# Kernel tuning notes

Hardware: AMD Instinct MI355X
Metric: run time of the kernel (lower is better)

## Reference

```python
import jax, jax.numpy as jnp
import numpy as np

B, T, D, S, K = 8, 4096, 1024, 64, 3
EPS = 1e-5

def setup_inputs() -> dict:
    key = jax.random.key(0)
    ks = jax.random.split(key, 10)
    def lin(k, out_d, in_d):
        s = 1.0 / np.sqrt(in_d)
        return jax.random.uniform(k, (out_d, in_d), jnp.float32, -s, s)
    return {
        "x": jax.random.normal(ks[0], (B, T, D), jnp.float32),
        "norm_w": jnp.ones((D,), jnp.float32),
        "norm_b": jnp.zeros((D,), jnp.float32),
        "in_w": lin(ks[1], 2 * D, D),
        "in_b": jnp.zeros((2 * D,), jnp.float32),
        "conv_w": jax.random.normal(ks[2], (D, 1, K), jnp.float32) / np.sqrt(K),
        "conv_b": jnp.zeros((D,), jnp.float32),
        "dt_w": lin(ks[3], S, D),
        "dt_b": jnp.zeros((S,), jnp.float32),
        "b_w": lin(ks[4], S, D),
        "b_b": jnp.zeros((S,), jnp.float32),
        "c_w": lin(ks[5], S, D),
        "c_b": jnp.zeros((S,), jnp.float32),
        "a_log": jax.random.normal(ks[6], (S,), jnp.float32) * 0.02,
        "d": jnp.ones((D,), jnp.float32),
        "out_w": lin(ks[7], D, D + S),
        "out_b": jnp.zeros((D,), jnp.float32),
    }

def reference(x, norm_w, norm_b, in_w, in_b, conv_w, conv_b,
              dt_w, dt_b, b_w, b_b, c_w, c_b, a_log, d, out_w, out_b):
    bsz, tlen, dim = x.shape
    sdim = a_log.shape[0]
    k = conv_w.shape[-1]
    residual = x
    # LayerNorm
    mu = jnp.mean(x, axis=-1, keepdims=True)
    var = jnp.mean(jnp.square(x - mu), axis=-1, keepdims=True)
    xn = (x - mu) * jax.lax.rsqrt(var + EPS) * norm_w + norm_b
    # in_proj and chunk
    h = xn @ in_w.T + in_b                       # (B,T,2D)
    x_proj, z = jnp.split(h, 2, axis=-1)         # each (B,T,D)
    # depthwise conv over time, 'same' padding
    xc = jax.lax.conv_general_dilated(
        x_proj.transpose(0, 2, 1), conv_w, (1,), [(k // 2, k // 2)],
        dimension_numbers=("NCH", "OIH", "NCH"), feature_group_count=dim)
    x_conv = jnp.tanh((xc + conv_b[None, :, None]).transpose(0, 2, 1))  # (B,T,D)
    # gate projections for all timesteps at once
    dt = jax.nn.softplus(z @ dt_w.T + dt_b) + 1e-4   # (B,T,S)
    b = jnp.tanh(z @ b_w.T + b_b)                    # (B,T,S)
    c = jnp.tanh(z @ c_w.T + c_b)                    # (B,T,S)
    a = -jnp.exp(a_log)                              # (S,)
    decay = jnp.exp(a * dt)                          # (B,T,S)
    # linear recurrence: state_t = state_{t-1} * decay_t + b_t
    def step(state, inp):
        dec_t, b_t = inp
        state = state * dec_t + b_t
        return state, state
    _, states = jax.lax.scan(step, jnp.zeros((bsz, sdim), x.dtype),
                             (decay.transpose(1, 0, 2), b.transpose(1, 0, 2)))
    states = states.transpose(1, 0, 2)               # (B,T,S)
    y = c * states
    mix = jnp.concatenate([x_conv * d, y], axis=-1)  # (B,T,D+S)
    out = mix @ out_w.T + out_b                      # (B,T,D)
    return residual + out
```

## Files before the change

### kernel.cpp

```cpp
#include <hip/hip_runtime.h>

#define TT 4096
#define DD 1024
#define NN 32768

typedef short s16x8 __attribute__((ext_vector_type(8)));
typedef float f32x4 __attribute__((ext_vector_type(4)));
typedef unsigned short ushort_t;

__device__ __forceinline__ unsigned short f2bf(float f) {
  unsigned u = __float_as_uint(f);
  u += 0x7FFFu + ((u >> 16) & 1u);
  return (unsigned short)(u >> 16);
}
__device__ __forceinline__ float bf2f(unsigned short h) {
  return __uint_as_float(((unsigned)h) << 16);
}
__device__ __forceinline__ void load_lds16(const void* g, void* l) {
  __builtin_amdgcn_global_load_lds(
      (const __attribute__((address_space(1))) unsigned int*)g,
      (__attribute__((address_space(3))) unsigned int*)l, 16, 0, 0);
}

__global__ __launch_bounds__(256)
void cvt_kernel(const float* __restrict__ s, ushort_t* __restrict__ d, int n) {
  int i = (blockIdx.x * 256 + threadIdx.x) * 4;
  if (i < n) {
    float4 v = *(const float4*)&s[i];
    ushort4 o; o.x = f2bf(v.x); o.y = f2bf(v.y); o.z = f2bf(v.z); o.w = f2bf(v.w);
    *(ushort4*)&d[i] = o;
  }
}

__global__ __launch_bounds__(256)
void w3pad_kernel(const float* __restrict__ dt_w, const float* __restrict__ b_w,
                  const float* __restrict__ c_w, ushort_t* __restrict__ w3) {
  int e = (blockIdx.x * 256 + threadIdx.x) * 4;
  int row = e >> 10, col = e & 1023;
  float4 v; v.x = 0.f; v.y = 0.f; v.z = 0.f; v.w = 0.f;
  if (row < 64)       v = *(const float4*)&dt_w[(row << 10) + col];
  else if (row < 128) v = *(const float4*)&b_w[((row - 64) << 10) + col];
  else if (row < 192) v = *(const float4*)&c_w[((row - 128) << 10) + col];
  ushort4 o; o.x = f2bf(v.x); o.y = f2bf(v.y); o.z = f2bf(v.z); o.w = f2bf(v.w);
  *(ushort4*)&w3[e] = o;
}

__global__ __launch_bounds__(256)
void tpose_kernel(const float* __restrict__ src, ushort_t* __restrict__ dst) {
  __shared__ float tile[64][65];
  int bx = blockIdx.x & 15, by = blockIdx.x >> 4;
  int tx = threadIdx.x & 63, ty0 = threadIdx.x >> 6;
  #pragma unroll
  for (int i = 0; i < 16; ++i) {
    int ty = ty0 * 16 + i;
    tile[ty][tx] = src[(size_t)(by * 64 + ty) * 1024 + bx * 64 + tx];
  }
  __syncthreads();
  #pragma unroll
  for (int i = 0; i < 16; ++i) {
    int ty = ty0 * 16 + i;
    dst[(size_t)(bx * 64 + ty) * 1024 + by * 64 + tx] = f2bf(tile[tx][ty]);
  }
}

__global__ void gbias_kernel(const float* __restrict__ dt_w, const float* __restrict__ b_w,
                             const float* __restrict__ c_w, const float* __restrict__ dt_b,
                             const float* __restrict__ b_b, const float* __restrict__ c_b,
                             const float* __restrict__ in_b, float* __restrict__ gb) {
  int i = blockIdx.x, lane = threadIdx.x;
  const float* wr = i < 64 ? dt_w + (size_t)i * 1024
                  : i < 128 ? b_w + (size_t)(i - 64) * 1024
                            : c_w + (size_t)(i - 128) * 1024;
  float s = 0.f;
  for (int j = lane; j < 1024; j += 64) s += wr[j] * in_b[1024 + j];
  #pragma unroll
  for (int off = 32; off; off >>= 1) s += __shfl_xor(s, off, 64);
  if (lane == 0) {
    float bb = i < 64 ? dt_b[i] : i < 128 ? b_b[i - 64] : c_b[i - 128];
    gb[i] = s + bb;
  }
}

__global__ __launch_bounds__(256)
void ln_kernel(const float* __restrict__ x, const float* __restrict__ w,
               const float* __restrict__ bv, ushort_t* __restrict__ xn)
{
  int row = blockIdx.x * 4 + (threadIdx.x >> 6);
  int lane = threadIdx.x & 63;
  const float* xr = x + (size_t)row * DD;
  float4 v[4];
  float s = 0.f, ss = 0.f;
  #pragma unroll
  for (int j = 0; j < 4; ++j) {
    v[j] = *(const float4*)&xr[j * 256 + lane * 4];
    s  += v[j].x + v[j].y + v[j].z + v[j].w;
    ss += v[j].x * v[j].x + v[j].y * v[j].y + v[j].z * v[j].z + v[j].w * v[j].w;
  }
  #pragma unroll
  for (int off = 32; off > 0; off >>= 1) {
    s  += __shfl_xor(s, off, 64);
    ss += __shfl_xor(ss, off, 64);
  }
  float mean = s * (1.f / 1024.f);
  float var  = ss * (1.f / 1024.f) - mean * mean;
  float rinv = rsqrtf(var + 1e-5f);
  #pragma unroll
  for (int j = 0; j < 4; ++j) {
    int c = j * 256 + lane * 4;
    float4 wv = *(const float4*)&w[c];
    float4 bb = *(const float4*)&bv[c];
    ushort4 o;
    o.x = f2bf((v[j].x - mean) * rinv * wv.x + bb.x);
    o.y = f2bf((v[j].y - mean) * rinv * wv.y + bb.y);
    o.z = f2bf((v[j].z - mean) * rinv * wv.z + bb.z);
    o.w = f2bf((v[j].w - mean) * rinv * wv.w + bb.w);
    *(ushort4*)&xn[(size_t)row * DD + c] = o;
  }
}

template<int EP>
__global__ __launch_bounds__(512, 2)
void gemm256(const ushort_t* __restrict__ A, const ushort_t* __restrict__ W,
             int M, int N, int K,
             const float* __restrict__ bias0,
             ushort_t* __restrict__ o0, ushort_t* __restrict__ o1)
{
  __shared__ ushort_t lds[65536];
  const int tid = threadIdx.x;
  const int lane = tid & 63;
  const int wid = tid >> 6;
  const int wr = wid >> 2;
  const int wc = wid & 3;
  const int lane15 = lane & 15;
  const int lgrp = lane >> 4;
  const int rsw = (lane15 & 7) << 4;
  const int ntn = N >> 8;
  int bid = blockIdx.x;
  { const int cpx = (int)gridDim.x >> 3; bid = (bid & 7) * cpx + (bid >> 3); }
  const int brow = (bid / ntn) << 8;
  const int bcol = (bid % ntn) << 8;
  const int nk = K >> 6;
  const int sRow = tid >> 3;
  const int sCol = (tid & 7) << 4;
  const char* ldsb = (const char*)lds;
  (void)M;

#define STG(bufb, isB, h, kt) do { \
    const int ktc_ = (kt) < nk ? (kt) : nk - 1; \
    const ushort_t* gsrc_ = (isB) ? W : A; \
    const int rowb_ = ((isB) ? bcol : brow) + (h) * 128; \
    _Pragma("unroll") \
    for (int j_ = 0; j_ < 2; ++j_) { \
      const int r_ = j_ * 64 + sRow; \
      load_lds16((const char*)(gsrc_ + (size_t)(rowb_ + r_) * K) + ktc_ * 128 + (sCol ^ ((r_ & 7) << 4)), \
                 (char*)lds + (bufb) * 65536 + (isB) * 32768 + (h) * 16384 + r_ * 128 + sCol); \
    } } while (0)

#define LDA_(bufb, m, kk) \
  (*(const s16x8*)(ldsb + (bufb) * 65536 + wr * 16384 + ((m) * 16 + lane15) * 128 + (((kk) * 64 + lgrp * 16) ^ rsw)))
#define LDB_(bufb, n, kk) \
  (*(const s16x8*)(ldsb + (bufb) * 65536 + 32768 + (wc >> 1) * 16384 + ((wc & 1) * 64 + (n) * 16 + lane15) * 128 + (((kk) * 64 + lgrp * 16) ^ rsw)))

#define BARR() asm volatile("s_barrier" ::: "memory")
#define VMW2() asm volatile("s_waitcnt vmcnt(2)" ::: "memory")
#define VMW4() asm volatile("s_waitcnt vmcnt(4)" ::: "memory")

#define RDA(dst, bufb, mh) do { \
    _Pragma("unroll") for (int kk = 0; kk < 2; ++kk) \
    _Pragma("unroll") for (int q = 0; q < 4; ++q) \
      dst[kk][q] = LDA_(bufb, (mh) * 4 + q, kk); } while (0)
#define RDB(dst, bufb, nh) do { \
    _Pragma("unroll") for (int kk = 0; kk < 2; ++kk) \
    _Pragma("unroll") for (int p = 0; p < 2; ++p) \
      dst[kk][p] = LDB_(bufb, (nh) * 2 + p, kk); } while (0)

#define MFMAQ(AF, BF, mh, nh) do { \
    __builtin_amdgcn_s_setprio(1); \
    _Pragma("unroll") for (int kk = 0; kk < 2; ++kk) \
    _Pragma("unroll") for (int q = 0; q < 4; ++q) \
    _Pragma("unroll") for (int p = 0; p < 2; ++p) \
      acc[(mh) * 4 + q][(nh) * 2 + p] = __builtin_amdgcn_mfma_f32_16x16x32_bf16( \
          AF[kk][q], BF[kk][p], acc[(mh) * 4 + q][(nh) * 2 + p], 0, 0, 0); \
    __builtin_amdgcn_s_setprio(0); } while (0)

  f32x4 acc[8][4];
  #pragma unroll
  for (int m = 0; m < 8; ++m) {
    #pragma unroll
    for (int n = 0; n < 4; ++n) acc[m][n] = (f32x4){0.f, 0.f, 0.f, 0.f};
  }
  s16x8 afP[2][4], afQ[2][4];
  s16x8 b0[2][2], b1[2][2];

  STG(0, 1, 0, 0); STG(0, 0, 0, 0); STG(0, 0, 1, 0); STG(0, 1, 1, 0);
  STG(1, 1, 0, 1); STG(1, 0, 0, 1);
  VMW4(); BARR();
  RDA(afP, 0, 0); RDB(b0, 0, 0);

  const int nIter = nk >> 1;
  for (int it = 0; it < nIter; ++it) {
    const int t0 = 2 * it;
    STG(1, 0, 1, t0 + 1);
    MFMAQ(afP, b0, 0, 0);
    RDB(b1, 0, 1); BARR();
    STG(1, 1, 1, t0 + 1);
    MFMAQ(afP, b1, 0, 1);
    RDA(afQ, 0, 1); BARR();
    STG(0, 1, 0, t0 + 2);
    MFMAQ(afQ, b1, 1, 1);
    VMW2(); BARR();
    STG(0, 0, 0, t0 + 2);
    MFMAQ(afQ, b0, 1, 0);
    RDA(afP, 1, 0); RDB(b1, 1, 1); BARR();
    STG(0, 0, 1, t0 + 2);
    MFMAQ(afP, b1, 0, 1);
    RDB(b0, 1, 0); BARR();
    STG(0, 1, 1, t0 + 2);
    MFMAQ(afP, b0, 0, 0);
    RDA(afQ, 1, 1); BARR();
    STG(1, 1, 0, t0 + 3);
    MFMAQ(afQ, b0, 1, 0);
    VMW2(); BARR();
    STG(1, 0, 0, t0 + 3);
    MFMAQ(afQ, b1, 1, 1);
    RDA(afP, 0, 0); RDB(b0, 0, 0); BARR();
  }
  if (nk & 1) {
    MFMAQ(afP, b0, 0, 0);
    RDB(b1, 0, 1);
    MFMAQ(afP, b1, 0, 1);
    RDA(afQ, 0, 1);
    MFMAQ(afQ, b1, 1, 1);
    MFMAQ(afQ, b0, 1, 0);
  }

#undef STG
#undef LDA_
#undef LDB_
#undef BARR
#undef VMW2
#undef VMW4
#undef RDA
#undef RDB
#undef MFMAQ

  #pragma unroll
  for (int m = 0; m < 8; ++m) {
    #pragma unroll
    for (int i = 0; i < 4; ++i) {
      const int r = brow + wr * 128 + m * 16 + lgrp * 4 + i;
      #pragma unroll
      for (int n = 0; n < 4; ++n) {
        const int col = bcol + wc * 64 + n * 16 + lane15;
        float v = acc[m][n][i] + bias0[col];
        if (col < DD) o0[(size_t)r * DD + col] = f2bf(v);
        else          o1[(size_t)r * DD + (col - DD)] = f2bf(v);
      }
    }
  }
}

__global__ __launch_bounds__(512, 4)
void gemm3_bk32(const ushort_t* __restrict__ A, const ushort_t* __restrict__ W,
                int M, int N, int K,
                const float* __restrict__ bias, const float* __restrict__ resid,
                float* __restrict__ outf)
{
  __shared__ ushort_t lds[24576];
  const int tid = threadIdx.x;
  const int lane = tid & 63;
  const int wid = tid >> 6;
  const int wr = wid >> 2;
  const int wc = wid & 3;
  const int lane15 = lane & 15;
  const int lgrp = lane >> 4;
  const int ntn = N >> 8;
  int bid = blockIdx.x;
  { const int cpx = (int)gridDim.x >> 3; bid = (bid & 7) * cpx + (bid >> 3); }
  const int brow = (bid / ntn) << 7;
  const int bcol = (bid % ntn) << 8;
  const int nk = K >> 5;
  const int sR = tid >> 2;
  const int sC = (tid & 3) << 4;
  const char* ldsb = (const char*)lds;
  (void)M;

  f32x4 acc[4][4];
  #pragma unroll
  for (int q = 0; q < 4; ++q)
    #pragma unroll
    for (int p = 0; p < 4; ++p) acc[q][p] = (f32x4){0.f, 0.f, 0.f, 0.f};

#define STG3(bufb, kt) do { \
    load_lds16((const char*)(A + (size_t)(brow + sR) * K + (kt) * 32) + sC, \
               (char*)lds + (bufb) * 24576 + sR * 64 + sC); \
    load_lds16((const char*)(W + (size_t)(bcol + sR) * K + (kt) * 32) + sC, \
               (char*)lds + (bufb) * 24576 + 8192 + sR * 64 + sC); \
    load_lds16((const char*)(W + (size_t)(bcol + 128 + sR) * K + (kt) * 32) + sC, \
               (char*)lds + (bufb) * 24576 + 8192 + (128 + sR) * 64 + sC); \
  } while (0)

  STG3(0, 0);
  __syncthreads();

  int cur = 0;
  for (int t = 0; t < nk; ++t) {
    if (t + 1 < nk) STG3(cur ^ 1, t + 1);
    s16x8 af[4], bf[4];
    #pragma unroll
    for (int q = 0; q < 4; ++q)
      af[q] = *(const s16x8*)(ldsb + cur * 24576 + (wr * 64 + q * 16 + lane15) * 64 + lgrp * 16);
    #pragma unroll
    for (int p = 0; p < 4; ++p)
      bf[p] = *(const s16x8*)(ldsb + cur * 24576 + 8192 + (wc * 64 + p * 16 + lane15) * 64 + lgrp * 16);
    __builtin_amdgcn_s_setprio(1);
    #pragma unroll
    for (int q = 0; q < 4; ++q)
      #pragma unroll
      for (int p = 0; p < 4; ++p)
        acc[q][p] = __builtin_amdgcn_mfma_f32_16x16x32_bf16(af[q], bf[p], acc[q][p], 0, 0, 0);
    __builtin_amdgcn_s_setprio(0);
    __syncthreads();
    cur ^= 1;
  }
#undef STG3

  #pragma unroll
  for (int q = 0; q < 4; ++q) {
    #pragma unroll
    for (int i = 0; i < 4; ++i) {
      const int r = brow + wr * 64 + q * 16 + lgrp * 4 + i;
      #pragma unroll
      for (int p = 0; p < 4; ++p) {
        const int col = bcol + wc * 64 + p * 16 + lane15;
        outf[(size_t)r * DD + col] = acc[q][p][i] + bias[col] + resid[(size_t)r * DD + col];
      }
    }
  }
}

__global__ __launch_bounds__(256)
void gemm128w(const ushort_t* __restrict__ A, const ushort_t* __restrict__ W,
              int M, int N, int K, ushort_t* __restrict__ o0)
{
  __shared__ ushort_t As[128 * 64];
  __shared__ ushort_t Bs[128 * 64];
  const int tid = threadIdx.x;
  const int lane = tid & 63;
  const int wid = tid >> 6;
  const int ntn = N >> 7;
  const int brow = (blockIdx.x / ntn) << 7;
  const int bcol = (blockIdx.x % ntn) << 7;
  const int wr = (wid >> 1) << 6;
  const int wc = (wid & 1) << 6;
  const int lane15 = lane & 15;
  const int lgrp = lane >> 4;
  (void)M;

  f32x4 acc[4][4];
  #pragma unroll
  for (int m = 0; m < 4; ++m)
    #pragma unroll
    for (int n = 0; n < 4; ++n)
      acc[m][n] = (f32x4){0.f, 0.f, 0.f, 0.f};

  const int r0 = tid >> 3;
  const int c0 = (tid & 7) << 3;
  const ushort_t* gA = A + (size_t)(brow + r0) * K + c0;
  const ushort_t* gW = W + (size_t)(bcol + r0) * K + c0;
  ushort_t* lA = &As[r0 * 64 + c0];
  ushort_t* lB = &Bs[r0 * 64 + c0];

  for (int k0 = 0; k0 < K; k0 += 64) {
    #pragma unroll
    for (int j = 0; j < 4; ++j) {
      load_lds16(gA + (size_t)(j * 32) * K + k0, lA + j * 32 * 64);
      load_lds16(gW + (size_t)(j * 32) * K + k0, lB + j * 32 * 64);
    }
    __syncthreads();
    #pragma unroll
    for (int kk = 0; kk < 2; ++kk) {
      s16x8 af[4], bfr[4];
      #pragma unroll
      for (int m = 0; m < 4; ++m)
        af[m] = *(const s16x8*)&As[(wr + m * 16 + lane15) * 64 + kk * 32 + lgrp * 8];
      #pragma unroll
      for (int n = 0; n < 4; ++n)
        bfr[n] = *(const s16x8*)&Bs[(wc + n * 16 + lane15) * 64 + kk * 32 + lgrp * 8];
      #pragma unroll
      for (int m = 0; m < 4; ++m)
        #pragma unroll
        for (int n = 0; n < 4; ++n)
          acc[m][n] = __builtin_amdgcn_mfma_f32_16x16x32_bf16(af[m], bfr[n], acc[m][n], 0, 0, 0);
    }
    __syncthreads();
  }

  #pragma unroll
  for (int m = 0; m < 4; ++m) {
    #pragma unroll
    for (int i = 0; i < 4; ++i) {
      const int r = brow + wr + m * 16 + lgrp * 4 + i;
      #pragma unroll
      for (int n = 0; n < 4; ++n) {
        const int col = bcol + wc + n * 16 + lane15;
        o0[(size_t)r * N + col] = f2bf(acc[m][n][i]);
      }
    }
  }
}

__global__ __launch_bounds__(256)
void gemm128g(const ushort_t* __restrict__ A, const ushort_t* __restrict__ W,
              int M, int N, int K,
              const float* __restrict__ gb, const float* __restrict__ alog,
              float* __restrict__ g0, float* __restrict__ g1, float* __restrict__ g2)
{
  __shared__ ushort_t As[128 * 64];
  __shared__ ushort_t Bs[128 * 64];
  const int tid = threadIdx.x;
  const int lane = tid & 63;
  const int wid = tid >> 6;
  const int ntn = N >> 7;
  const int brow = (blockIdx.x / ntn) << 7;
  const int bcol = (blockIdx.x % ntn) << 7;
  const int wr = (wid >> 1) << 6;
  const int wc = (wid & 1) << 6;
  const int lane15 = lane & 15;
  const int lgrp = lane >> 4;
  (void)M;

  f32x4 acc[4][4];
  #pragma unroll
  for (int m = 0; m < 4; ++m)
    #pragma unroll
    for (int n = 0; n < 4; ++n)
      acc[m][n] = (f32x4){0.f, 0.f, 0.f, 0.f};

  const int r0 = tid >> 3;
  const int c0 = (tid & 7) << 3;
  const ushort_t* gA = A + (size_t)(brow + r0) * K + c0;
  const ushort_t* gW = W + (size_t)(bcol + r0) * K + c0;
  ushort_t* lA = &As[r0 * 64 + c0];
  ushort_t* lB = &Bs[r0 * 64 + c0];

  for (int k0 = 0; k0 < K; k0 += 64) {
    #pragma unroll
    for (int j = 0; j < 4; ++j) {
      load_lds16(gA + (size_t)(j * 32) * K + k0, lA + j * 32 * 64);
      load_lds16(gW + (size_t)(j * 32) * K + k0, lB + j * 32 * 64);
    }
    __syncthreads();
    #pragma unroll
    for (int kk = 0; kk < 2; ++kk) {
      s16x8 af[4], bfr[4];
      #pragma unroll
      for (int m = 0; m < 4; ++m)
        af[m] = *(const s16x8*)&As[(wr + m * 16 + lane15) * 64 + kk * 32 + lgrp * 8];
      #pragma unroll
      for (int n = 0; n < 4; ++n)
        bfr[n] = *(const s16x8*)&Bs[(wc + n * 16 + lane15) * 64 + kk * 32 + lgrp * 8];
      #pragma unroll
      for (int m = 0; m < 4; ++m)
        #pragma unroll
        for (int n = 0; n < 4; ++n)
          acc[m][n] = __builtin_amdgcn_mfma_f32_16x16x32_bf16(af[m], bfr[n], acc[m][n], 0, 0, 0);
    }
    __syncthreads();
  }

  #pragma unroll
  for (int m = 0; m < 4; ++m) {
    #pragma unroll
    for (int i = 0; i < 4; ++i) {
      const int r = brow + wr + m * 16 + lgrp * 4 + i;
      #pragma unroll
      for (int n = 0; n < 4; ++n) {
        const int col = bcol + wc + n * 16 + lane15;
        float v = acc[m][n][i];
        if (col < 64) {
          float u = v + gb[col];
          float sp = (u > 20.f) ? u : log1pf(expf(u));
          g0[(size_t)r * 64 + col] = expf(-expf(alog[col]) * (sp + 1e-4f));
        } else if (col < 128) {
          g1[(size_t)r * 64 + (col - 64)] = tanhf(v + gb[col]);
        } else if (col < 192) {
          g2[(size_t)r * 64 + (col - 128)] = tanhf(v + gb[col]);
        }
      }
    }
  }
}

__global__ __launch_bounds__(256)
void conv_kernel(const ushort_t* __restrict__ xp, const float* __restrict__ cw,
                 const float* __restrict__ cb, const float* __restrict__ dvec,
                 ushort_t* __restrict__ mix)
{
  int idx = blockIdx.x * 256 + threadIdx.x;
  int row = idx >> 7;
  int d0 = (idx & 127) << 3;
  int t = row & (TT - 1);
  s16x8 cur = *(const s16x8*)&xp[(size_t)row * DD + d0];
  s16x8 prv; s16x8 nxt;
  #pragma unroll
  for (int j = 0; j < 8; ++j) { prv[j] = 0; nxt[j] = 0; }
  if (t > 0)      prv = *(const s16x8*)&xp[(size_t)(row - 1) * DD + d0];
  if (t < TT - 1) nxt = *(const s16x8*)&xp[(size_t)(row + 1) * DD + d0];
  float wv[24];
  #pragma unroll
  for (int j = 0; j < 6; ++j) *(float4*)&wv[j * 4] = *(const float4*)&cw[d0 * 3 + j * 4];
  float cbv[8], dv[8];
  *(float4*)&cbv[0] = *(const float4*)&cb[d0];
  *(float4*)&cbv[4] = *(const float4*)&cb[d0 + 4];
  *(float4*)&dv[0]  = *(const float4*)&dvec[d0];
  *(float4*)&dv[4]  = *(const float4*)&dvec[d0 + 4];
  s16x8 o;
  #pragma unroll
  for (int j = 0; j < 8; ++j) {
    float acc = cbv[j] + bf2f((ushort_t)prv[j]) * wv[j * 3]
              + bf2f((ushort_t)cur[j]) * wv[j * 3 + 1]
              + bf2f((ushort_t)nxt[j]) * wv[j * 3 + 2];
    o[j] = (short)f2bf(tanhf(acc) * dv[j]);
  }
  *(s16x8*)&mix[(size_t)row * 1088 + d0] = o;
}

__global__ void scanA_kernel(const float* __restrict__ dec, const float* __restrict__ bb,
                             float* __restrict__ P, float* __restrict__ Q)
{
  int b = blockIdx.x >> 6, ci = blockIdx.x & 63, s = threadIdx.x;
  size_t base = (((size_t)b * TT) + ci * 64) * 64 + s;
  float p = 1.f, q = 0.f;
  #pragma unroll 4
  for (int t = 0; t < 64; ++t) {
    float d = dec[base + (size_t)t * 64];
    float w = bb[base + (size_t)t * 64];
    q = q * d + w; p *= d;
  }
  int o = (b * 64 + ci) * 64 + s;
  P[o] = p; Q[o] = q;
}

__global__ void scanB_kernel(const float* __restrict__ P, const float* __restrict__ Q,
                             float* __restrict__ I)
{
  int b = blockIdx.x, s = threadIdx.x;
  float st = 0.f;
  for (int ci = 0; ci < 64; ++ci) {
    int o = (b * 64 + ci) * 64 + s;
    I[o] = st;
    st = st * P[o] + Q[o];
  }
}

__global__ void scanC_kernel(const float* __restrict__ dec, const float* __restrict__ bb,
                             const float* __restrict__ cc, const float* __restrict__ I,
                             ushort_t* __restrict__ mix)
{
  int b = blockIdx.x >> 6, ci = blockIdx.x & 63, s = threadIdx.x;
  size_t base = (((size_t)b * TT) + ci * 64) * 64 + s;
  float st = I[(b * 64 + ci) * 64 + s];
  size_t mrow = (size_t)b * TT + ci * 64;
  #pragma unroll 4
  for (int t = 0; t < 64; ++t) {
    size_t o = base + (size_t)t * 64;
    st = st * dec[o] + bb[o];
    mix[(mrow + t) * 1088 + 1024 + s] = (ushort_t)f2bf(cc[o] * st);
  }
}

extern "C" void kernel_launch(void* const* d_in, const int* in_sizes, int n_in,
                              void* d_out, int out_size, void* d_ws, size_t ws_size,
                              hipStream_t stream)
{
  (void)in_sizes; (void)n_in; (void)out_size; (void)ws_size;
  const float* x      = (const float*)d_in[0];
  const float* norm_w = (const float*)d_in[1];
  const float* norm_b = (const float*)d_in[2];
  const float* in_w   = (const float*)d_in[3];
  const float* in_b   = (const float*)d_in[4];
  const float* conv_w = (const float*)d_in[5];
  const float* conv_b = (const float*)d_in[6];
  const float* dt_w   = (const float*)d_in[7];
  const float* dt_b   = (const float*)d_in[8];
  const float* b_w    = (const float*)d_in[9];
  const float* b_b    = (const float*)d_in[10];
  const float* c_w    = (const float*)d_in[11];
  const float* c_b    = (const float*)d_in[12];
  const float* a_log  = (const float*)d_in[13];
  const float* dvec   = (const float*)d_in[14];
  const float* out_w  = (const float*)d_in[15];
  const float* out_b  = (const float*)d_in[16];
  float* out = (float*)d_out;

  char* p = (char*)d_ws;
  ushort_t* mix    = (ushort_t*)p;
  ushort_t* xn     = mix;
  p += 71303168;
  ushort_t* xproj  = (ushort_t*)p; p += 67108864;
  char*     zreg   = p;            p += 67108864;
  ushort_t* w1_bf  = (ushort_t*)p; p += 4194304;
  ushort_t* w3     = (ushort_t*)p; p += 524288;
  ushort_t* outw_bf= (ushort_t*)p; p += 2228224;
  float* P = (float*)p; p += 131072;
  float* Q = (float*)p; p += 131072;
  float* I = (float*)p; p += 131072;

  float* gdec = (float*)zreg;
  float* gbb  = (float*)(zreg + 8388608);
  float* gcc  = (float*)(zreg + 16777216);
  ushort_t* inw2t  = (ushort_t*)(zreg + 33554432);
  float*    gb     = (float*)(zreg + 37748736);
  ushort_t* wgates = (ushort_t*)(zreg + 41943040);

  cvt_kernel<<<1024, 256, 0, stream>>>(in_w, w1_bf, 1048576);
  cvt_kernel<<<1088, 256, 0, stream>>>(out_w, outw_bf, 1114112);
  tpose_kernel<<<256, 256, 0, stream>>>(in_w + 1048576, inw2t);
  w3pad_kernel<<<256, 256, 0, stream>>>(dt_w, b_w, c_w, w3);
  gemm128w<<<16, 256, 0, stream>>>(w3, inw2t, 256, 1024, 1024, wgates);
  gbias_kernel<<<192, 64, 0, stream>>>(dt_w, b_w, c_w, dt_b, b_b, c_b, in_b, gb);

  ln_kernel<<<8192, 256, 0, stream>>>(x, norm_w, norm_b, xn);

  gemm256<0><<<(NN / 256) * (1024 / 256), 512, 0, stream>>>(
      xn, w1_bf, NN, 1024, 1024, in_b, xproj, nullptr);

  gemm128g<<<(NN / 128) * (256 / 128), 256, 0, stream>>>(
      xn, wgates, NN, 256, 1024, gb, a_log, gdec, gbb, gcc);

  conv_kernel<<<NN * 128 / 256, 256, 0, stream>>>(xproj, conv_w, conv_b, dvec, mix);

  scanA_kernel<<<512, 64, 0, stream>>>(gdec, gbb, P, Q);
  scanB_kernel<<<8, 64, 0, stream>>>(P, Q, I);
  scanC_kernel<<<512, 64, 0, stream>>>(gdec, gbb, gcc, I, mix);

  gemm3_bk32<<<(NN / 128) * (1024 / 256), 512, 0, stream>>>(
      mix, outw_bf, NN, 1024, 1088, out_b, x, out);
}
```

Before: 398.0 us.

## Rework out-projection GEMM to 128x128 tiles, BK=64 and XOR-swizzled LDS

Replaces the 512-thread 128x256 BK=32 out-projection GEMM with a 256-thread 128x128 tile kernel using BK=64 and an XOR swizzle on LDS rows, applied on the global-read side so the LDS writes stay linear. This halves the number of k-iterations and barriers and aims to remove LDS bank conflicts on the fragment reads. The grid doubles in block count while each block does less work. K=1088 is divisible by 64, so the loop count stays exact. The smaller tile means less operand reuse per block, and occupancy changes from 4 to 2 blocks per CU.

```diff
diff --git a/kernel.cpp b/kernel.cpp
--- a/kernel.cpp
+++ b/kernel.cpp
@@ -260,28 +260,29 @@
   }
 }
 
-__global__ __launch_bounds__(512, 4)
-void gemm3_bk32(const ushort_t* __restrict__ A, const ushort_t* __restrict__ W,
-                int M, int N, int K,
-                const float* __restrict__ bias, const float* __restrict__ resid,
-                float* __restrict__ outf)
-{
-  __shared__ ushort_t lds[24576];
+__global__ __launch_bounds__(256, 2)
+void gemm3_128(const ushort_t* __restrict__ A, const ushort_t* __restrict__ W,
+               int M, int N, int K,
+               const float* __restrict__ bias, const float* __restrict__ resid,
+               float* __restrict__ outf)
+{
+  __shared__ ushort_t lds[32768];
   const int tid = threadIdx.x;
   const int lane = tid & 63;
   const int wid = tid >> 6;
-  const int wr = wid >> 2;
-  const int wc = wid & 3;
+  const int wr = wid >> 1;
+  const int wc = wid & 1;
   const int lane15 = lane & 15;
   const int lgrp = lane >> 4;
-  const int ntn = N >> 8;
+  const int rsw = (lane15 & 7) << 4;
+  const int ntn = N >> 7;
   int bid = blockIdx.x;
   { const int cpx = (int)gridDim.x >> 3; bid = (bid & 7) * cpx + (bid >> 3); }
   const int brow = (bid / ntn) << 7;
-  const int bcol = (bid % ntn) << 8;
-  const int nk = K >> 5;
-  const int sR = tid >> 2;
-  const int sC = (tid & 3) << 4;
+  const int bcol = (bid % ntn) << 7;
+  const int nk = K >> 6;
+  const int sRow = tid >> 3;
+  const int sCol = (tid & 7) << 4;
   const char* ldsb = (const char*)lds;
   (void)M;
 
@@ -292,13 +293,14 @@
     for (int p = 0; p < 4; ++p) acc[q][p] = (f32x4){0.f, 0.f, 0.f, 0.f};
 
 #define STG3(bufb, kt) do { \
-    load_lds16((const char*)(A + (size_t)(brow + sR) * K + (kt) * 32) + sC, \
-               (char*)lds + (bufb) * 24576 + sR * 64 + sC); \
-    load_lds16((const char*)(W + (size_t)(bcol + sR) * K + (kt) * 32) + sC, \
-               (char*)lds + (bufb) * 24576 + 8192 + sR * 64 + sC); \
-    load_lds16((const char*)(W + (size_t)(bcol + 128 + sR) * K + (kt) * 32) + sC, \
-               (char*)lds + (bufb) * 24576 + 8192 + (128 + sR) * 64 + sC); \
-  } while (0)
+    _Pragma("unroll") \
+    for (int j_ = 0; j_ < 4; ++j_) { \
+      const int r_ = j_ * 32 + sRow; \
+      load_lds16((const char*)(A + (size_t)(brow + r_) * K) + (kt) * 128 + (sCol ^ ((r_ & 7) << 4)), \
+                 (char*)lds + (bufb) * 32768 + r_ * 128 + sCol); \
+      load_lds16((const char*)(W + (size_t)(bcol + r_) * K) + (kt) * 128 + (sCol ^ ((r_ & 7) << 4)), \
+                 (char*)lds + (bufb) * 32768 + 16384 + r_ * 128 + sCol); \
+    } } while (0)
 
   STG3(0, 0);
   __syncthreads();
@@ -306,20 +308,25 @@
   int cur = 0;
   for (int t = 0; t < nk; ++t) {
     if (t + 1 < nk) STG3(cur ^ 1, t + 1);
-    s16x8 af[4], bf[4];
-    #pragma unroll
-    for (int q = 0; q < 4; ++q)
-      af[q] = *(const s16x8*)(ldsb + cur * 24576 + (wr * 64 + q * 16 + lane15) * 64 + lgrp * 16);
-    #pragma unroll
-    for (int p = 0; p < 4; ++p)
-      bf[p] = *(const s16x8*)(ldsb + cur * 24576 + 8192 + (wc * 64 + p * 16 + lane15) * 64 + lgrp * 16);
-    __builtin_amdgcn_s_setprio(1);
-    #pragma unroll
-    for (int q = 0; q < 4; ++q)
+    #pragma unroll
+    for (int kk = 0; kk < 2; ++kk) {
+      s16x8 af[4], bf[4];
+      #pragma unroll
+      for (int q = 0; q < 4; ++q)
+        af[q] = *(const s16x8*)(ldsb + cur * 32768 +
+                 (wr * 64 + q * 16 + lane15) * 128 + ((kk * 64 + lgrp * 16) ^ rsw));
       #pragma unroll
       for (int p = 0; p < 4; ++p)
-        acc[q][p] = __builtin_amdgcn_mfma_f32_16x16x32_bf16(af[q], bf[p], acc[q][p], 0, 0, 0);
-    __builtin_amdgcn_s_setprio(0);
+        bf[p] = *(const s16x8*)(ldsb + cur * 32768 + 16384 +
+                 (wc * 64 + p * 16 + lane15) * 128 + ((kk * 64 + lgrp * 16) ^ rsw));
+      __builtin_amdgcn_s_setprio(1);
+      #pragma unroll
+      for (int q = 0; q < 4; ++q)
+        #pragma unroll
+        for (int p = 0; p < 4; ++p)
+          acc[q][p] = __builtin_amdgcn_mfma_f32_16x16x32_bf16(af[q], bf[p], acc[q][p], 0, 0, 0);
+      __builtin_amdgcn_s_setprio(0);
+    }
     __syncthreads();
     cur ^= 1;
   }
@@ -635,6 +642,6 @@
   scanB_kernel<<<8, 64, 0, stream>>>(P, Q, I);
   scanC_kernel<<<512, 64, 0, stream>>>(gdec, gbb, gcc, I, mix);
 
-  gemm3_bk32<<<(NN / 128) * (1024 / 256), 512, 0, stream>>>(
+  gemm3_128<<<(NN / 128) * (1024 / 128), 256, 0, stream>>>(
       mix, outw_bf, NN, 1024, 1088, out_b, x, out);
 }
```

Result: no change. 392.7 us (-1.3%).
